# Performance work log

Hardware: AMD Instinct MI355X
Metric: run time of the kernel (lower is better)

## Reference

```python
import jax, jax.numpy as jnp
import numpy as np

EPS = 1e-5
SLOPE = 0.2


def _conv_bn_lrelu(x, w, b, g, be, m, v):
    # 1x1 conv: (B,C,H,W) x (O,C) -> (B,O,H,W), then BN (inference) + LeakyReLU(0.2)
    y = jnp.einsum('bchw,oc->bohw', x, w) + b[None, :, None, None]
    y = g[None, :, None, None] * (y - m[None, :, None, None]) * jax.lax.rsqrt(v[None, :, None, None] + EPS) + be[None, :, None, None]
    return jnp.where(y >= 0, y, SLOPE * y)


def setup_inputs() -> dict:
    key = jax.random.key(0)
    ks = jax.random.split(key, 20)
    B, C, H, W = 8, 64, 256, 256
    d = {}
    d['x'] = jax.random.normal(ks[0], (B, C, H, W), dtype=jnp.float32)
    d['w1'] = jax.random.normal(ks[1], (1, C), dtype=jnp.float32) * 0.1
    d['b1'] = jax.random.normal(ks[2], (1,), dtype=jnp.float32)
    d['g1'] = jax.random.uniform(ks[3], (1,), dtype=jnp.float32) + 0.5
    d['be1'] = jax.random.normal(ks[4], (1,), dtype=jnp.float32)
    d['m1'] = jax.random.normal(ks[5], (1,), dtype=jnp.float32)
    d['v1'] = jax.random.uniform(ks[6], (1,), dtype=jnp.float32) + 0.5
    d['wA'] = jax.random.normal(ks[7], (C, C), dtype=jnp.float32) * 0.1
    d['bA'] = jax.random.normal(ks[8], (C,), dtype=jnp.float32)
    d['gA'] = jax.random.uniform(ks[9], (C,), dtype=jnp.float32) + 0.5
    d['beA'] = jax.random.normal(ks[10], (C,), dtype=jnp.float32)
    d['mA'] = jax.random.normal(ks[11], (C,), dtype=jnp.float32)
    d['vA'] = jax.random.uniform(ks[12], (C,), dtype=jnp.float32) + 0.5
    d['wO'] = jax.random.normal(ks[13], (C, C), dtype=jnp.float32) * 0.1
    d['bO'] = jax.random.normal(ks[14], (C,), dtype=jnp.float32)
    d['gO'] = jax.random.uniform(ks[15], (C,), dtype=jnp.float32) + 0.5
    d['beO'] = jax.random.normal(ks[16], (C,), dtype=jnp.float32)
    d['mO'] = jax.random.normal(ks[17], (C,), dtype=jnp.float32)
    d['vO'] = jax.random.uniform(ks[18], (C,), dtype=jnp.float32) + 0.5
    return d


def reference(x, w1, b1, g1, be1, m1, v1, wA, bA, gA, beA, mA, vA, wO, bO, gO, beO, mO, vO):
    B, C, H, W = x.shape
    # Branch 1: C->1 conv + BN + LeakyReLU, squeeze channel -> (B,H,W)
    C1 = _conv_bn_lrelu(x, w1, b1, g1, be1, m1, v1)[:, 0]  # (B,H,W)
    C1_t = jnp.swapaxes(C1, 1, 2)                           # (B,W,H)
    S1 = jax.nn.softmax(jnp.matmul(C1, C1_t), axis=-1)      # (B,H,H)
    S2 = jax.nn.softmax(jnp.matmul(C1_t, C1), axis=-1)      # (B,W,W)
    # Branch 2: C->C conv + BN + LeakyReLU
    C2 = _conv_bn_lrelu(x, wA, bA, gA, beA, mA, vA)         # (B,C,H,W)
    # Raw row-major reshapes as in the torch code (mixes channel and spatial dims)
    R1 = C2.reshape(B, H, C * W)
    R2 = C2.reshape(B, W, C * H)
    R3 = jnp.matmul(S1, R1).reshape(B, C, H, W)
    R4 = jnp.matmul(S2, R2).reshape(B, C, H, W)
    C3 = _conv_bn_lrelu(R3 + R4, wO, bO, gO, beO, mO, vO)
    out = C2 + C3
    return (out, S1, S2)
```

## Files before the change

### kernel.cpp

```cpp
#include <hip/hip_runtime.h>


#define EPS 1e-5f

typedef __attribute__((ext_vector_type(8))) short bf16x8;
typedef __attribute__((ext_vector_type(4))) float f32x4;

__device__ __forceinline__ unsigned short f2bf(float f){
  union { float f; unsigned int u; } a; a.f = f;
  return (unsigned short)((a.u + 0x7fffu + ((a.u >> 16) & 1u)) >> 16);
}
__device__ __forceinline__ float lrelu(float y){ return y >= 0.f ? y : 0.2f * y; }
__device__ __forceinline__ bf16x8 cvt8(const float* p){
  float4 a = *(const float4*)p;
  float4 b = *(const float4*)(p + 4);
  bf16x8 r;
  r[0] = (short)f2bf(a.x); r[1] = (short)f2bf(a.y); r[2] = (short)f2bf(a.z); r[3] = (short)f2bf(a.w);
  r[4] = (short)f2bf(b.x); r[5] = (short)f2bf(b.y); r[6] = (short)f2bf(b.z); r[7] = (short)f2bf(b.w);
  return r;
}

__global__ __launch_bounds__(256) void k1_c1(
    const float* __restrict__ x, const float* __restrict__ w1,
    const float* __restrict__ pb1, const float* __restrict__ pg1,
    const float* __restrict__ pbe1, const float* __restrict__ pm1,
    const float* __restrict__ pv1,
    float* __restrict__ C1)
{
  const int blk = blockIdx.x;
  const int b = blk >> 6;
  const int n0 = (blk & 63) << 10;
  const int t = threadIdx.x;
  __shared__ float w1s[64];
  if (t < 64) w1s[t] = w1[t];
  __syncthreads();
  const float* xb = x + ((size_t)b << 22);
  const int n = n0 + (t << 2);
  float4 d = {0.f, 0.f, 0.f, 0.f};
  #pragma unroll 8
  for (int c = 0; c < 64; c++){
    const float4 xv = *(const float4*)(xb + ((size_t)c << 16) + n);
    const float wv = w1s[c];
    d.x = fmaf(xv.x, wv, d.x); d.y = fmaf(xv.y, wv, d.y);
    d.z = fmaf(xv.z, wv, d.z); d.w = fmaf(xv.w, wv, d.w);
  }
  const float s1 = pg1[0] * rsqrtf(pv1[0] + EPS);
  const float t1 = (pb1[0] - pm1[0]) * s1 + pbe1[0];
  float4 o;
  o.x = lrelu(d.x * s1 + t1); o.y = lrelu(d.y * s1 + t1);
  o.z = lrelu(d.z * s1 + t1); o.w = lrelu(d.w * s1 + t1);
  *(float4*)(C1 + (b << 16) + n) = o;
}

__global__ __launch_bounds__(256) void k2_gram(const float* __restrict__ C1, float* __restrict__ G)
{
  const int bx = blockIdx.x;
  const int b = bx >> 5;
  const int which = (bx >> 4) & 1;
  const int tile = bx & 15;
  const int i0 = (tile >> 2) << 6, j0 = (tile & 3) << 6;
  const float* Cb = C1 + (b << 16);
  __shared__ float Al[32][68];
  __shared__ float Bl[32][68];
  const int t = threadIdx.x;
  const int tx = t & 15, ty = t >> 4;
  float acc[4][4];
  #pragma unroll
  for (int i = 0; i < 4; i++)
    #pragma unroll
    for (int j = 0; j < 4; j++) acc[i][j] = 0.f;

  for (int kc = 0; kc < 8; kc++){
    const int k0 = kc << 5;
    __syncthreads();
    if (which == 0){
      const int i = t & 63, kq = t >> 6;
      const float* pa = Cb + (i0 + i)*256 + k0 + kq*8;
      const float* pb = Cb + (j0 + i)*256 + k0 + kq*8;
      #pragma unroll
      for (int u = 0; u < 8; u++){ Al[kq*8+u][i] = pa[u]; Bl[kq*8+u][i] = pb[u]; }
    } else {
      const int k = t >> 3, i8 = (t & 7) << 3;
      const float* pa = Cb + (k0 + k)*256 + i0 + i8;
      const float* pb = Cb + (k0 + k)*256 + j0 + i8;
      *(float4*)&Al[k][i8]   = *(const float4*)pa;
      *(float4*)&Al[k][i8+4] = *(const float4*)(pa+4);
      *(float4*)&Bl[k][i8]   = *(const float4*)pb;
      *(float4*)&Bl[k][i8+4] = *(const float4*)(pb+4);
    }
    __syncthreads();
    #pragma unroll 4
    for (int k = 0; k < 32; k++){
      float4 a4 = *(const float4*)&Al[k][ty << 2];
      float4 b4 = *(const float4*)&Bl[k][tx << 2];
      float av[4] = {a4.x, a4.y, a4.z, a4.w};
      float bw[4] = {b4.x, b4.y, b4.z, b4.w};
      #pragma unroll
      for (int ii = 0; ii < 4; ii++)
        #pragma unroll
        for (int jj = 0; jj < 4; jj++)
          acc[ii][jj] = fmaf(av[ii], bw[jj], acc[ii][jj]);
    }
  }
  float* Go = G + ((size_t)(which*8 + b) << 16);
  #pragma unroll
  for (int r = 0; r < 4; r++){
    float4 o4 = {acc[r][0], acc[r][1], acc[r][2], acc[r][3]};
    *(float4*)&Go[(i0 + (ty<<2) + r)*256 + j0 + (tx<<2)] = o4;
  }
}

__global__ __launch_bounds__(256) void k2_softmax(const float* __restrict__ G,
    float* __restrict__ S1o, float* __restrict__ S2o,
    unsigned short* __restrict__ Ssum2)
{
  const int bx = blockIdx.x;
  const int b = bx >> 8, i = bx & 255;
  const int j = threadIdx.x;
  const float v1 = G[((size_t)b << 16) + i*256 + j];
  const float v2 = G[((size_t)(8 + b) << 16) + i*256 + j];
  __shared__ float sm[4], sm2[4], ss[4], ss2[4];
  float a1 = v1, a2 = v2;
  #pragma unroll
  for (int off = 32; off > 0; off >>= 1){
    a1 = fmaxf(a1, __shfl_xor(a1, off));
    a2 = fmaxf(a2, __shfl_xor(a2, off));
  }
  const int wv = j >> 6;
  if ((j & 63) == 0){ sm[wv] = a1; sm2[wv] = a2; }
  __syncthreads();
  const float m1v = fmaxf(fmaxf(sm[0], sm[1]), fmaxf(sm[2], sm[3]));
  const float m2v = fmaxf(fmaxf(sm2[0], sm2[1]), fmaxf(sm2[2], sm2[3]));
  float e1 = __expf(v1 - m1v), e2 = __expf(v2 - m2v);
  float s1 = e1, s2 = e2;
  #pragma unroll
  for (int off = 32; off > 0; off >>= 1){
    s1 += __shfl_xor(s1, off);
    s2 += __shfl_xor(s2, off);
  }
  if ((j & 63) == 0){ ss[wv] = s1; ss2[wv] = s2; }
  __syncthreads();
  const float d1 = ss[0]+ss[1]+ss[2]+ss[3];
  const float d2 = ss2[0]+ss2[1]+ss2[2]+ss2[3];
  const float S1v = e1 / d1, S2v = e2 / d2;
  S1o[((size_t)b << 16) + i*256 + j] = S1v;
  S2o[((size_t)b << 16) + i*256 + j] = S2v;
  const int ip = ((i & 3) << 6) | (i >> 2);
  const int kp = ((j & 3) << 6) | (j >> 2);
  Ssum2[((size_t)b << 16) + ip*256 + kp] = f2bf(S1v + S2v);
}

__global__ __launch_bounds__(256, 2) void k3_main(
    const float* __restrict__ x,
    const float* __restrict__ wA, const float* __restrict__ pbA,
    const float* __restrict__ pgA, const float* __restrict__ pbeA,
    const float* __restrict__ pmA, const float* __restrict__ pvA,
    const unsigned short* __restrict__ Ssum2,
    const float* __restrict__ wO, const float* __restrict__ pbO,
    const float* __restrict__ pgO, const float* __restrict__ pbeO,
    const float* __restrict__ pmO, const float* __restrict__ pvO,
    float* __restrict__ out)
{
  __shared__ unsigned short C2L[256][72];
  __shared__ unsigned short T_lds[256][72];
  __shared__ float sAl[64], tAl[64], sOl[64], tOl[64];
  const int blk = blockIdx.x;
  const int b  = blk >> 8;
  const int j0 = (blk & 255) << 6;
  const int t = threadIdx.x;
  const int lane = t & 63, wv = t >> 6;
  const int m = lane & 15, q = lane >> 4;

  if (t < 64){
    const float sA = pgA[t] * rsqrtf(pvA[t] + EPS);
    sAl[t] = sA; tAl[t] = (pbA[t] - pmA[t]) * sA + pbeA[t];
    const float sO = pgO[t] * rsqrtf(pvO[t] + EPS);
    sOl[t] = sO; tOl[t] = (pbO[t] - pmO[t]) * sO + pbeO[t];
  }
  __syncthreads();

  float sAv[4], tAv[4];
  #pragma unroll
  for (int ot = 0; ot < 4; ot++){ sAv[ot] = sAl[16*ot + m]; tAv[ot] = tAl[16*ot + m]; }

  bf16x8 wfrA[4][2];
  #pragma unroll
  for (int ot = 0; ot < 4; ot++)
    #pragma unroll
    for (int ks = 0; ks < 2; ks++)
      wfrA[ot][ks] = cvt8(wA + (16*ot + m)*64 + ks*32 + q*8);

  const f32x4 vzero = {0.f, 0.f, 0.f, 0.f};
  f32x4 c2r[4][4];
  #pragma unroll
  for (int i = 0; i < 4; i++)
    #pragma unroll
    for (int j = 0; j < 4; j++) c2r[i][j] = vzero;

  const float* xb = x + ((size_t)b << 22) + (wv << 14) + j0;
  #pragma unroll
  for (int ks = 0; ks < 2; ks++)
    #pragma unroll
    for (int nt = 0; nt < 4; nt++){
      bf16x8 af;
      #pragma unroll
      for (int u = 0; u < 8; u++){
        const int cin = ks*32 + q*8 + u;
        af[u] = (short)f2bf(xb[((size_t)cin << 16) + 16*nt + m]);
      }
      #pragma unroll
      for (int ot = 0; ot < 4; ot++)
        c2r[nt][ot] = __builtin_amdgcn_mfma_f32_16x16x32_bf16(af, wfrA[ot][ks], c2r[nt][ot], 0, 0, 0);
    }

  #pragma unroll
  for (int nt = 0; nt < 4; nt++)
    #pragma unroll
    for (int ot = 0; ot < 4; ot++){
      #pragma unroll
      for (int r = 0; r < 4; r++){
        const float v = lrelu(c2r[nt][ot][r] * sAv[ot] + tAv[ot]);
        c2r[nt][ot][r] = v;
        C2L[64*wv + 16*nt + 4*q + r][16*ot + m] = f2bf(v);
      }
    }
  __syncthreads();

  const unsigned short* Sb = Ssum2 + ((size_t)b << 16);
  f32x4 accT[4][4];
  #pragma unroll
  for (int i = 0; i < 4; i++)
    #pragma unroll
    for (int j = 0; j < 4; j++) accT[i][j] = vzero;

  #pragma unroll
  for (int ks = 0; ks < 8; ks++){
    const int kk = ks*32 + q*8;
    const int rk = kk >> 6;
    const int c0 = kk & 63;
    bf16x8 af[4], bv[4];
    #pragma unroll
    for (int it = 0; it < 4; it++)
      af[it] = *(const bf16x8*)(Sb + (64*wv + 16*it + m)*256 + kk);
    #pragma unroll
    for (int jt = 0; jt < 4; jt++)
      bv[jt] = *(const bf16x8*)&C2L[(rk << 6) + 16*jt + m][c0];
    #pragma unroll
    for (int it = 0; it < 4; it++)
      #pragma unroll
      for (int jt = 0; jt < 4; jt++)
        accT[it][jt] = __builtin_amdgcn_mfma_f32_16x16x32_bf16(af[it], bv[jt], accT[it][jt], 0, 0, 0);
  }

  #pragma unroll
  for (int it = 0; it < 4; it++)
    #pragma unroll
    for (int jt = 0; jt < 4; jt++){
      uint2 pk;
      pk.x = (unsigned)f2bf(accT[it][jt][0]) | ((unsigned)f2bf(accT[it][jt][1]) << 16);
      pk.y = (unsigned)f2bf(accT[it][jt][2]) | ((unsigned)f2bf(accT[it][jt][3]) << 16);
      *(uint2*)&T_lds[64*wv + 16*jt + m][16*it + 4*q] = pk;
    }

  bf16x8 wfrO[4][2];
  #pragma unroll
  for (int ct = 0; ct < 4; ct++)
    #pragma unroll
    for (int k2 = 0; k2 < 2; k2++)
      wfrO[ct][k2] = cvt8(wO + (16*ct + m)*64 + k2*32 + q*8);

  f32x4 acc2[4][4];
  #pragma unroll
  for (int i = 0; i < 4; i++)
    #pragma unroll
    for (int j = 0; j < 4; j++) acc2[i][j] = vzero;

  #pragma unroll
  for (int k2 = 0; k2 < 2; k2++)
    #pragma unroll
    for (int stl = 0; stl < 4; stl++){
      const bf16x8 afT = *(const bf16x8*)&T_lds[64*wv + 16*stl + m][k2*32 + q*8];
      #pragma unroll
      for (int ct = 0; ct < 4; ct++)
        acc2[stl][ct] = __builtin_amdgcn_mfma_f32_16x16x32_bf16(afT, wfrO[ct][k2], acc2[stl][ct], 0, 0, 0);
    }

  float sOv[4], tOv[4];
  #pragma unroll
  for (int ct = 0; ct < 4; ct++){ sOv[ct] = sOl[16*ct + m]; tOv[ct] = tOl[16*ct + m]; }

  const size_t outB = ((size_t)b << 22);
  #pragma unroll
  for (int stl = 0; stl < 4; stl++)
    #pragma unroll
    for (int ct = 0; ct < 4; ct++){
      const int cout = 16*ct + m;
      const int ng0 = (wv << 14) + j0 + 16*stl + 4*q;
      float* po = out + outB + ((size_t)cout << 16) + ng0;
      float4 pk;
      pk.x = c2r[stl][ct][0] + lrelu(acc2[stl][ct][0] * sOv[ct] + tOv[ct]);
      pk.y = c2r[stl][ct][1] + lrelu(acc2[stl][ct][1] * sOv[ct] + tOv[ct]);
      pk.z = c2r[stl][ct][2] + lrelu(acc2[stl][ct][2] * sOv[ct] + tOv[ct]);
      pk.w = c2r[stl][ct][3] + lrelu(acc2[stl][ct][3] * sOv[ct] + tOv[ct]);
      *(float4*)po = pk;
    }
}

extern "C" void kernel_launch(void* const* d_in, const int* in_sizes, int n_in,
                              void* d_out, int out_size, void* d_ws, size_t ws_size,
                              hipStream_t stream) {
  const float* x   = (const float*)d_in[0];
  const float* w1  = (const float*)d_in[1];
  const float* b1  = (const float*)d_in[2];
  const float* g1  = (const float*)d_in[3];
  const float* be1 = (const float*)d_in[4];
  const float* m1  = (const float*)d_in[5];
  const float* v1  = (const float*)d_in[6];
  const float* wA  = (const float*)d_in[7];
  const float* bA  = (const float*)d_in[8];
  const float* gA  = (const float*)d_in[9];
  const float* beA = (const float*)d_in[10];
  const float* mA  = (const float*)d_in[11];
  const float* vA  = (const float*)d_in[12];
  const float* wO  = (const float*)d_in[13];
  const float* bO  = (const float*)d_in[14];
  const float* gO  = (const float*)d_in[15];
  const float* beO = (const float*)d_in[16];
  const float* mO  = (const float*)d_in[17];
  const float* vO  = (const float*)d_in[18];

  float* out = (float*)d_out;

  char* ws = (char*)d_ws;
  float* C1             = (float*)(ws);
  float* G              = (float*)(ws + (size_t)(2u << 20));
  unsigned short* Ssum2 = (unsigned short*)(ws + (size_t)(6u << 20));

  k1_c1<<<dim3(512), dim3(256), 0, stream>>>(x, w1, b1, g1, be1, m1, v1, C1);
  k2_gram<<<dim3(256), dim3(256), 0, stream>>>(C1, G);
  k2_softmax<<<dim3(2048), dim3(256), 0, stream>>>(G, out + 33554432u, out + 34078720u, Ssum2);
  k3_main<<<dim3(2048), dim3(256), 0, stream>>>(x, wA, bA, gA, beA, mA, vA, Ssum2,
                                                wO, bO, gO, beO, mO, vO, out);
}
```

Before: 364.0 us.

## Compute Gram matrices with split-bf16 MFMA and reuse output buffer as scratch

```diff
diff --git a/kernel.cpp b/kernel.cpp
--- a/kernel.cpp
+++ b/kernel.cpp
@@ -9,6 +9,9 @@
 __device__ __forceinline__ unsigned short f2bf(float f){
   union { float f; unsigned int u; } a; a.f = f;
   return (unsigned short)((a.u + 0x7fffu + ((a.u >> 16) & 1u)) >> 16);
+}
+__device__ __forceinline__ float bf2f(unsigned short u){
+  union { unsigned int i; float f; } v; v.i = ((unsigned int)u) << 16; return v.f;
 }
 __device__ __forceinline__ float lrelu(float y){ return y >= 0.f ? y : 0.2f * y; }
 __device__ __forceinline__ bf16x8 cvt8(const float* p){
@@ -25,7 +28,8 @@
     const float* __restrict__ pb1, const float* __restrict__ pg1,
     const float* __restrict__ pbe1, const float* __restrict__ pm1,
     const float* __restrict__ pv1,
-    float* __restrict__ C1)
+    unsigned short* __restrict__ C1hi, unsigned short* __restrict__ C1lo,
+    unsigned short* __restrict__ C1Thi, unsigned short* __restrict__ C1Tlo)
 {
   const int blk = blockIdx.x;
   const int b = blk >> 6;
@@ -37,7 +41,7 @@
   const float* xb = x + ((size_t)b << 22);
   const int n = n0 + (t << 2);
   float4 d = {0.f, 0.f, 0.f, 0.f};
-  #pragma unroll 8
+  #pragma unroll 16
   for (int c = 0; c < 64; c++){
     const float4 xv = *(const float4*)(xb + ((size_t)c << 16) + n);
     const float wv = w1s[c];
@@ -46,68 +50,89 @@
   }
   const float s1 = pg1[0] * rsqrtf(pv1[0] + EPS);
   const float t1 = (pb1[0] - pm1[0]) * s1 + pbe1[0];
-  float4 o;
-  o.x = lrelu(d.x * s1 + t1); o.y = lrelu(d.y * s1 + t1);
-  o.z = lrelu(d.z * s1 + t1); o.w = lrelu(d.w * s1 + t1);
-  *(float4*)(C1 + (b << 16) + n) = o;
-}
-
-__global__ __launch_bounds__(256) void k2_gram(const float* __restrict__ C1, float* __restrict__ G)
+  float o[4];
+  o[0] = lrelu(d.x * s1 + t1); o[1] = lrelu(d.y * s1 + t1);
+  o[2] = lrelu(d.z * s1 + t1); o[3] = lrelu(d.w * s1 + t1);
+
+  unsigned short hi[4], lo[4];
+  #pragma unroll
+  for (int e = 0; e < 4; e++){
+    hi[e] = f2bf(o[e]);
+    lo[e] = f2bf(o[e] - bf2f(hi[e]));
+  }
+  const int base = (b << 16) + n;
+  uint2 ph, pl;
+  ph.x = (unsigned)hi[0] | ((unsigned)hi[1] << 16);
+  ph.y = (unsigned)hi[2] | ((unsigned)hi[3] << 16);
+  pl.x = (unsigned)lo[0] | ((unsigned)lo[1] << 16);
+  pl.y = (unsigned)lo[2] | ((unsigned)lo[3] << 16);
+  *(uint2*)(C1hi + base) = ph;
+  *(uint2*)(C1lo + base) = pl;
+  const int h = n >> 8, w = n & 255;
+  #pragma unroll
+  for (int e = 0; e < 4; e++){
+    C1Thi[(b << 16) + (w + e)*256 + h] = hi[e];
+    C1Tlo[(b << 16) + (w + e)*256 + h] = lo[e];
+  }
+}
+
+__global__ __launch_bounds__(256) void k2_gram(
+    const unsigned short* __restrict__ C1hi, const unsigned short* __restrict__ C1lo,
+    const unsigned short* __restrict__ C1Thi, const unsigned short* __restrict__ C1Tlo,
+    float* __restrict__ G)
 {
   const int bx = blockIdx.x;
+  const int tile = bx & 15;
+  const int which = (bx >> 4) & 1;
   const int b = bx >> 5;
-  const int which = (bx >> 4) & 1;
-  const int tile = bx & 15;
-  const int i0 = (tile >> 2) << 6, j0 = (tile & 3) << 6;
-  const float* Cb = C1 + (b << 16);
-  __shared__ float Al[32][68];
-  __shared__ float Bl[32][68];
   const int t = threadIdx.x;
-  const int tx = t & 15, ty = t >> 4;
-  float acc[4][4];
-  #pragma unroll
-  for (int i = 0; i < 4; i++)
-    #pragma unroll
-    for (int j = 0; j < 4; j++) acc[i][j] = 0.f;
-
-  for (int kc = 0; kc < 8; kc++){
-    const int k0 = kc << 5;
-    __syncthreads();
-    if (which == 0){
-      const int i = t & 63, kq = t >> 6;
-      const float* pa = Cb + (i0 + i)*256 + k0 + kq*8;
-      const float* pb = Cb + (j0 + i)*256 + k0 + kq*8;
-      #pragma unroll
-      for (int u = 0; u < 8; u++){ Al[kq*8+u][i] = pa[u]; Bl[kq*8+u][i] = pb[u]; }
-    } else {
-      const int k = t >> 3, i8 = (t & 7) << 3;
-      const float* pa = Cb + (k0 + k)*256 + i0 + i8;
-      const float* pb = Cb + (k0 + k)*256 + j0 + i8;
-      *(float4*)&Al[k][i8]   = *(const float4*)pa;
-      *(float4*)&Al[k][i8+4] = *(const float4*)(pa+4);
-      *(float4*)&Bl[k][i8]   = *(const float4*)pb;
-      *(float4*)&Bl[k][i8+4] = *(const float4*)(pb+4);
-    }
-    __syncthreads();
-    #pragma unroll 4
-    for (int k = 0; k < 32; k++){
-      float4 a4 = *(const float4*)&Al[k][ty << 2];
-      float4 b4 = *(const float4*)&Bl[k][tx << 2];
-      float av[4] = {a4.x, a4.y, a4.z, a4.w};
-      float bw[4] = {b4.x, b4.y, b4.z, b4.w};
-      #pragma unroll
-      for (int ii = 0; ii < 4; ii++)
-        #pragma unroll
-        for (int jj = 0; jj < 4; jj++)
-          acc[ii][jj] = fmaf(av[ii], bw[jj], acc[ii][jj]);
-    }
-  }
+  const int lane = t & 63, wv = t >> 6;
+  const int m = lane & 15, q = lane >> 4;
+  const int ibase = ((tile >> 2) << 6) + 32*(wv >> 1);
+  const int jbase = ((tile & 3) << 6) + 32*(wv & 1);
+
+  const unsigned short* Phi = (which ? C1Thi : C1hi) + ((size_t)b << 16);
+  const unsigned short* Plo = (which ? C1Tlo : C1lo) + ((size_t)b << 16);
+
+  const f32x4 vzero = {0.f, 0.f, 0.f, 0.f};
+  f32x4 acc[2][2];
+  #pragma unroll
+  for (int i = 0; i < 2; i++)
+    #pragma unroll
+    for (int j = 0; j < 2; j++) acc[i][j] = vzero;
+
+  #pragma unroll
+  for (int ks = 0; ks < 8; ks++){
+    const int kk = ks*32 + q*8;
+    bf16x8 ah[2], al[2], bh[2], bl[2];
+    #pragma unroll
+    for (int it = 0; it < 2; it++){
+      ah[it] = *(const bf16x8*)(Phi + (ibase + 16*it + m)*256 + kk);
+      al[it] = *(const bf16x8*)(Plo + (ibase + 16*it + m)*256 + kk);
+    }
+    #pragma unroll
+    for (int jt = 0; jt < 2; jt++){
+      bh[jt] = *(const bf16x8*)(Phi + (jbase + 16*jt + m)*256 + kk);
+      bl[jt] = *(const bf16x8*)(Plo + (jbase + 16*jt + m)*256 + kk);
+    }
+    #pragma unroll
+    for (int it = 0; it < 2; it++)
+      #pragma unroll
+      for (int jt = 0; jt < 2; jt++){
+        acc[it][jt] = __builtin_amdgcn_mfma_f32_16x16x32_bf16(ah[it], bh[jt], acc[it][jt], 0, 0, 0);
+        acc[it][jt] = __builtin_amdgcn_mfma_f32_16x16x32_bf16(ah[it], bl[jt], acc[it][jt], 0, 0, 0);
+        acc[it][jt] = __builtin_amdgcn_mfma_f32_16x16x32_bf16(al[it], bh[jt], acc[it][jt], 0, 0, 0);
+      }
+  }
+
   float* Go = G + ((size_t)(which*8 + b) << 16);
   #pragma unroll
-  for (int r = 0; r < 4; r++){
-    float4 o4 = {acc[r][0], acc[r][1], acc[r][2], acc[r][3]};
-    *(float4*)&Go[(i0 + (ty<<2) + r)*256 + j0 + (tx<<2)] = o4;
-  }
+  for (int it = 0; it < 2; it++)
+    #pragma unroll
+    for (int jt = 0; jt < 2; jt++)
+      #pragma unroll
+      for (int r = 0; r < 4; r++)
+        Go[(ibase + 16*it + 4*q + r)*256 + jbase + 16*jt + m] = acc[it][jt][r];
 }
 
 __global__ __launch_bounds__(256) void k2_softmax(const float* __restrict__ G,
@@ -161,7 +186,7 @@
     const float* __restrict__ pmO, const float* __restrict__ pvO,
     float* __restrict__ out)
 {
-  __shared__ unsigned short C2L[256][72];
+  __shared__ unsigned short XL[256][72];
   __shared__ unsigned short T_lds[256][72];
   __shared__ float sAl[64], tAl[64], sOl[64], tOl[64];
   const int blk = blockIdx.x;
@@ -205,8 +230,8 @@
       bf16x8 af;
       #pragma unroll
       for (int u = 0; u < 8; u++){
-        const int cin = ks*32 + q*8 + u;
-        af[u] = (short)f2bf(xb[((size_t)cin << 16) + 16*nt + m]);
+        const int c = ks*32 + q*8 + u;
+        af[u] = (short)f2bf(xb[((size_t)c << 16) + 16*nt + m]);
       }
       #pragma unroll
       for (int ot = 0; ot < 4; ot++)
@@ -221,7 +246,7 @@
       for (int r = 0; r < 4; r++){
         const float v = lrelu(c2r[nt][ot][r] * sAv[ot] + tAv[ot]);
         c2r[nt][ot][r] = v;
-        C2L[64*wv + 16*nt + 4*q + r][16*ot + m] = f2bf(v);
+        XL[64*wv + 16*nt + 4*q + r][16*ot + m] = f2bf(v);
       }
     }
   __syncthreads();
@@ -244,7 +269,7 @@
       af[it] = *(const bf16x8*)(Sb + (64*wv + 16*it + m)*256 + kk);
     #pragma unroll
     for (int jt = 0; jt < 4; jt++)
-      bv[jt] = *(const bf16x8*)&C2L[(rk << 6) + 16*jt + m][c0];
+      bv[jt] = *(const bf16x8*)&XL[(rk << 6) + 16*jt + m][c0];
     #pragma unroll
     for (int it = 0; it < 4; it++)
       #pragma unroll
@@ -332,13 +357,16 @@
   float* out = (float*)d_out;
 
   char* ws = (char*)d_ws;
-  float* C1             = (float*)(ws);
-  float* G              = (float*)(ws + (size_t)(2u << 20));
+  unsigned short* C1hi  = (unsigned short*)(ws);
+  unsigned short* C1lo  = (unsigned short*)(ws + (size_t)(1u << 20));
+  unsigned short* C1Thi = (unsigned short*)(ws + (size_t)(2u << 20));
+  unsigned short* C1Tlo = (unsigned short*)(ws + (size_t)(3u << 20));
   unsigned short* Ssum2 = (unsigned short*)(ws + (size_t)(6u << 20));
 
-  k1_c1<<<dim3(512), dim3(256), 0, stream>>>(x, w1, b1, g1, be1, m1, v1, C1);
-  k2_gram<<<dim3(256), dim3(256), 0, stream>>>(C1, G);
-  k2_softmax<<<dim3(2048), dim3(256), 0, stream>>>(G, out + 33554432u, out + 34078720u, Ssum2);
+  k1_c1<<<dim3(512), dim3(256), 0, stream>>>(x, w1, b1, g1, be1, m1, v1,
+                                             C1hi, C1lo, C1Thi, C1Tlo);
+  k2_gram<<<dim3(256), dim3(256), 0, stream>>>(C1hi, C1lo, C1Thi, C1Tlo, out);
+  k2_softmax<<<dim3(2048), dim3(256), 0, stream>>>(out, out + 33554432u, out + 34078720u, Ssum2);
   k3_main<<<dim3(2048), dim3(256), 0, stream>>>(x, wA, bA, gA, beA, mA, vA, Ssum2,
                                                 wO, bO, gO, beO, mO, vO, out);
 }
```

Result: no change. 366.1 us (+0.6%).
